# Kernel optimization log

Hardware: AMD Instinct MI355X
Metric: run time of the kernel (lower is better)

Reference implementation:

```python
import jax, jax.numpy as jnp
import numpy as np
import math

L, K, B = 16, 2048, 2
BATCH = 4
N = K * B


def _pe(k, b_beats):
    # PositionalEncoding buffer: pe[features_dim=K, num_of_beats=B]
    pos = jnp.arange(k, dtype=jnp.float32)[:, None]                      # (K, 1)
    div = jnp.exp(jnp.arange(0, b_beats, 2, dtype=jnp.float32) * (-math.log(10000.0) / b_beats))
    pe = jnp.zeros((k, b_beats), dtype=jnp.float32)
    pe = pe.at[:, 0::2].set(jnp.sin(pos * div))
    pe = pe.at[:, 1::2].set(jnp.cos(pos * div))
    return pe                                                            # (K, B)


def setup_inputs() -> dict:
    key = jax.random.key(0)
    ks = jax.random.split(key, 10)
    return {
        "X": jax.random.normal(ks[0], (BATCH, L, N), jnp.float32),
        "S": jax.random.normal(ks[1], (BATCH, L, N), jnp.float32),
        "W_1x": jax.random.normal(ks[2], (L, L), jnp.float32),
        "W_1s": jax.random.normal(ks[3], (L, L), jnp.float32),
        "W_2x": jax.random.normal(ks[4], (K, K), jnp.float32),
        "W_2s": jax.random.normal(ks[5], (K, K), jnp.float32),
        "conv_wx": jax.random.normal(ks[6], (2 * L, 2 * L, 3, 3), jnp.float32) * 0.05,
        "conv_bx": jnp.zeros((2 * L,), jnp.float32),
        "conv_ws": jax.random.normal(ks[7], (2 * L, 2 * L, 3, 3), jnp.float32) * 0.05,
        "conv_bs": jnp.zeros((2 * L,), jnp.float32),
    }


def _branch(E, W2):
    # E: (b, L, N). A = softmax(E^T E, axis=2); Ea = E @ A; then K-dim mixing by W2.
    b = E.shape[0]
    A = jax.nn.softmax(jnp.einsum('bln,blm->bnm', E, E), axis=2)         # (b, N, N)
    Ea = jnp.einsum('bln,bnm->blm', E, A)                                # (b, L, N)
    Ea4 = Ea.reshape(b, L, K, B)
    M = jnp.einsum('blkt,kj->bljt', Ea4, W2)                             # (b, L, K, B)
    return M.reshape(b, L, N)


def _conv(x, w, bias):
    y = jax.lax.conv_general_dilated(x, w, (1, 1), 'SAME',
                                     dimension_numbers=('NCHW', 'OIHW', 'NCHW'))
    return y + bias[None, :, None, None]


def reference(X, S, W_1x, W_1s, W_2x, W_2s, conv_wx, conv_bx, conv_ws, conv_bs):
    b = X.shape[0]
    Xe = jnp.einsum('bln,lm->bmn', S, W_1x)
    Se = jnp.einsum('bln,lm->bmn', X, W_1s)
    Mx = _branch(Xe, W_2x)
    Ms = _branch(Se, W_2s)
    X_hat = jnp.concatenate((Mx * X, X), axis=1).reshape(b, 2 * L, K, B)
    S_hat = jnp.concatenate((Ms * S, S), axis=1).reshape(b, 2 * L, K, B)
    # positional encoding broadcast over (batch, 2L); dropout in eval mode = identity
    S_hat = S_hat + _pe(K, B)[None, None]
    X_e_hat = _conv(X_hat, conv_wx, conv_bx)
    S_e_hat = _conv(S_hat, conv_ws, conv_bs)
    return jnp.concatenate((X_e_hat, S_e_hat), axis=1)                   # (b, 4L, K, B)
```

## Files before the change

### kernel.cpp

```cpp
#include <hip/hip_runtime.h>
#include <math.h>

#define TPB 256

static constexpr int LL = 16;
static constexpr int KK = 2048;
static constexpr int NBATCH = 4;
static constexpr int NN = 4096;
static constexpr int BBR = 8;

static constexpr size_t OFF_EHL = 0;
static constexpr size_t OFF_ET  = 524288;
static constexpr size_t OFF_LSE = 786432;
static constexpr size_t OFF_EAT = 819200;
static constexpr size_t OFF_XH  = 1081344;
static constexpr size_t OFF_SH  = 1605632;
static constexpr size_t OFF_PB  = 2129920;
static constexpr size_t OFF_PMX = 3178496;
static constexpr size_t OFF_PSM = 3244032;

typedef unsigned short ushortT;
typedef __attribute__((ext_vector_type(8))) short short8v;
typedef __attribute__((ext_vector_type(4))) float f32x4;

__device__ __forceinline__ ushortT f2bf(float x) {
  union { float f; unsigned int u; } c; c.f = x;
  unsigned int u = c.u;
  return (ushortT)((u + 0x7FFFu + ((u >> 16) & 1u)) >> 16);
}
__device__ __forceinline__ float bf2f(ushortT h) {
  union { unsigned int u; float f; } c; c.u = ((unsigned int)h) << 16;
  return c.f;
}
__device__ __forceinline__ float exp2a(float x) {
  float r; asm("v_exp_f32 %0, %1" : "=v"(r) : "v"(x)); return r;
}

__global__ __launch_bounds__(TPB) void prep_kernel(
    const float* __restrict__ X, const float* __restrict__ S,
    const float* __restrict__ W1x, const float* __restrict__ W1s,
    ushortT* __restrict__ Ehl, ushortT* __restrict__ Ept) {
  __shared__ float wsh[256];
  __shared__ ushortT tl[16][272];
  const int tid = threadIdx.x;
  const int br = blockIdx.z;
  wsh[tid] = br ? W1s[tid] : W1x[tid];
  __syncthreads();
  const int n0 = blockIdx.x * 256;
  const int b = blockIdx.y;
  const int n = n0 + tid;
  const float SC = 1.2011224087f;
  const int wq = tid & 31;
  const int slot = (wq < 16) ? ((wq >> 2) * 8 + (wq & 3))
                             : (((wq - 16) >> 2) * 8 + 4 + (wq & 3));
  const int ptid = (tid & ~31) | slot;
  const float* In = br ? X : S;

  float in[16];
#pragma unroll
  for (int l = 0; l < 16; ++l)
    in[l] = In[(size_t)(b * 16 + l) * NN + n];
  float e[16];
#pragma unroll
  for (int m = 0; m < 16; ++m) {
    float a0 = 0.f;
#pragma unroll
    for (int l = 0; l < 16; ++l) a0 = fmaf(in[l], wsh[l * 16 + m], a0);
    e[m] = a0;
  }
  const int bbr = br * 4 + b;
  unsigned int rw[16];
#pragma unroll
  for (int q = 0; q < 16; ++q) rw[q] = 0;
#pragma unroll
  for (int k = 0; k < 16; ++k) {
    const float vs = e[k] * SC;
    ushortT h = f2bf(vs);
    ushortT lo = f2bf(vs - bf2f(h));
    rw[k >> 1] |= ((unsigned int)h) << (16 * (k & 1));
    rw[8 + (k >> 1)] |= ((unsigned int)lo) << (16 * (k & 1));
    tl[k][ptid] = f2bf(e[k]);
  }
  uint4* dst = (uint4*)(Ehl + ((size_t)bbr * NN + n) * 32);
  dst[0] = make_uint4(rw[0], rw[1], rw[2], rw[3]);
  dst[1] = make_uint4(rw[4], rw[5], rw[6], rw[7]);
  dst[2] = make_uint4(rw[8], rw[9], rw[10], rw[11]);
  dst[3] = make_uint4(rw[12], rw[13], rw[14], rw[15]);
  __syncthreads();
  {
    const int r = tid >> 4, c0 = (tid & 15) * 16;
    const uint4* src = (const uint4*)(&tl[r][c0]);
    uint4* d2 = (uint4*)(Ept + ((size_t)bbr * 16 + r) * NN + n0 + c0);
    d2[0] = src[0];
    d2[1] = src[1];
  }
}

__global__ __launch_bounds__(TPB) void passA_kernel(
    const ushortT* __restrict__ Ehl, float* __restrict__ pmx,
    float* __restrict__ psm) {
  const int bid = blockIdx.x;
  const int bbr = bid & 7;
  const int ms = (bid >> 3) & 1;
  const int n0 = (bid >> 4) * 32;
  const int tid = threadIdx.x;
  const int w = tid >> 6, lane = tid & 63;
  const int lr = lane & 15, g = lane >> 4;
  const ushortT* Eb = Ehl + (size_t)bbr * NN * 32;

  const short8v zero8 = {0, 0, 0, 0, 0, 0, 0, 0};
  short8v b1[2], b2[2];
#pragma unroll
  for (int s = 0; s < 2; ++s) {
    const ushortT* rp = Eb + (size_t)(n0 + s * 16 + lr) * 32;
    b1[s] = *(const short8v*)(rp + (g & 1) * 8);
    b2[s] = zero8;
    if (g < 2) b2[s] = *(const short8v*)(rp + 16 + g * 8);
  }
  float mx[2] = {-INFINITY, -INFINITY};
  float sm[2] = {0.f, 0.f};
  const f32x4 z = {0.f, 0.f, 0.f, 0.f};
  const ushortT* ap = Eb + (size_t)(ms * 2048 + w * 512 + lr) * 32 + g * 8;
#pragma unroll 2
  for (int ch = 0; ch < 16; ++ch) {
    short8v a0 = *(const short8v*)ap;
    short8v a1 = *(const short8v*)(ap + 16 * 32);
    ap += 32 * 32;
#pragma unroll
    for (int s = 0; s < 2; ++s) {
      f32x4 c0 = __builtin_amdgcn_mfma_f32_16x16x32_bf16(a0, b1[s], z, 0, 0, 0);
      c0 = __builtin_amdgcn_mfma_f32_16x16x32_bf16(a0, b2[s], c0, 0, 0, 0);
      f32x4 c1 = __builtin_amdgcn_mfma_f32_16x16x32_bf16(a1, b1[s], z, 0, 0, 0);
      c1 = __builtin_amdgcn_mfma_f32_16x16x32_bf16(a1, b2[s], c1, 0, 0, 0);
      float t0 = fmaxf(fmaxf(c0[0], c0[1]), fmaxf(c0[2], c0[3]));
      float t1 = fmaxf(fmaxf(c1[0], c1[1]), fmaxf(c1[2], c1[3]));
      float tm = fmaxf(t0, t1);
      if (tm > mx[s] + 30.f) {
        sm[s] *= exp2a(mx[s] - tm);
        mx[s] = tm;
      }
      float e0 = exp2a(c0[0] - mx[s]), e1 = exp2a(c0[1] - mx[s]);
      float e2 = exp2a(c0[2] - mx[s]), e3 = exp2a(c0[3] - mx[s]);
      float e4 = exp2a(c1[0] - mx[s]), e5 = exp2a(c1[1] - mx[s]);
      float e6 = exp2a(c1[2] - mx[s]), e7 = exp2a(c1[3] - mx[s]);
      sm[s] += ((e0 + e1) + (e2 + e3)) + ((e4 + e5) + (e6 + e7));
    }
  }
#pragma unroll
  for (int s = 0; s < 2; ++s) {
    for (int off = 16; off < 64; off <<= 1) {
      float omx = __shfl_xor(mx[s], off);
      float osm = __shfl_xor(sm[s], off);
      float nm = fmaxf(mx[s], omx);
      sm[s] = sm[s] * exp2a(mx[s] - nm) + osm * exp2a(omx - nm);
      mx[s] = nm;
    }
  }
  __shared__ float smx[4][2][16], ssm[4][2][16];
  if (lane < 16) {
    smx[w][0][lr] = mx[0]; ssm[w][0][lr] = sm[0];
    smx[w][1][lr] = mx[1]; ssm[w][1][lr] = sm[1];
  }
  __syncthreads();
  if (tid < 32) {
    const int s = tid >> 4, col = tid & 15;
    float M = fmaxf(fmaxf(smx[0][s][col], smx[1][s][col]),
                    fmaxf(smx[2][s][col], smx[3][s][col]));
    float Ssum = ssm[0][s][col] * exp2a(smx[0][s][col] - M) +
                 ssm[1][s][col] * exp2a(smx[1][s][col] - M) +
                 ssm[2][s][col] * exp2a(smx[2][s][col] - M) +
                 ssm[3][s][col] * exp2a(smx[3][s][col] - M);
    const size_t o = (size_t)(ms * 8 + bbr) * NN + n0 + s * 16 + col;
    pmx[o] = M;
    psm[o] = Ssum;
  }
}

__global__ __launch_bounds__(TPB) void reduceA_kernel(
    const float* __restrict__ pmx, const float* __restrict__ psm,
    float* __restrict__ nlse) {
  const int idx = blockIdx.x * TPB + threadIdx.x;
  float m0 = pmx[idx], m1 = pmx[32768 + idx];
  float s0 = psm[idx], s1 = psm[32768 + idx];
  float M = fmaxf(m0, m1);
  float S = s0 * exp2a(m0 - M) + s1 * exp2a(m1 - M);
  nlse[idx] = -(M + log2f(fmaxf(S, 1e-38f)));
}

__global__ __launch_bounds__(TPB) void passB_kernel(
    const ushortT* __restrict__ Ehl, const ushortT* __restrict__ Ept,
    const float* __restrict__ nlse, float* __restrict__ pb) {
  const int bid = blockIdx.x;
  const int bbr = bid & 7;
  const int ns = (bid >> 3) & 1;
  const int m0 = (bid >> 4) * 64;
  const int tid = threadIdx.x;
  const int w = tid >> 6, lane = tid & 63;
  const int lr = lane & 15, g = lane >> 4;
  const ushortT* Eb = Ehl + (size_t)bbr * NN * 32;
  const ushortT* Tb = Ept + (size_t)bbr * 16 * NN;
  __shared__ float lsb[2048];
  __shared__ float red[4][4][16][17];
  for (int i = tid; i < 2048; i += TPB)
    lsb[i] = nlse[(size_t)bbr * NN + ns * 2048 + i];
  __syncthreads();

  const short8v zero8 = {0, 0, 0, 0, 0, 0, 0, 0};
  short8v b1[4], b2[4];
#pragma unroll
  for (int s = 0; s < 4; ++s) {
    const ushortT* rp = Eb + (size_t)(m0 + s * 16 + lr) * 32;
    b1[s] = *(const short8v*)(rp + (g & 1) * 8);
    b2[s] = zero8;
    if (g < 2) b2[s] = *(const short8v*)(rp + 16 + g * 8);
  }
  f32x4 acc[4] = {{0.f, 0.f, 0.f, 0.f}, {0.f, 0.f, 0.f, 0.f},
                  {0.f, 0.f, 0.f, 0.f}, {0.f, 0.f, 0.f, 0.f}};
  const ushortT* ap = Eb + (size_t)(ns * 2048 + w * 512 + lr) * 32 + g * 8;
  const ushortT* vp = Tb + (size_t)lr * NN + ns * 2048 + w * 512 + g * 8;
  const float* lp = lsb + w * 512 + g * 4;
#pragma unroll 2
  for (int ch = 0; ch < 16; ++ch) {
    short8v a0 = *(const short8v*)ap;
    short8v a1 = *(const short8v*)(ap + 16 * 32);
    short8v ae = *(const short8v*)vp;
    f32x4 sd0 = *(const f32x4*)lp;
    f32x4 sd1 = *(const f32x4*)(lp + 16);
    ap += 32 * 32; vp += 32; lp += 32;
#pragma unroll
    for (int s = 0; s < 4; ++s) {
      f32x4 c0 = __builtin_amdgcn_mfma_f32_16x16x32_bf16(a0, b1[s], sd0, 0, 0, 0);
      c0 = __builtin_amdgcn_mfma_f32_16x16x32_bf16(a0, b2[s], c0, 0, 0, 0);
      f32x4 c1 = __builtin_amdgcn_mfma_f32_16x16x32_bf16(a1, b1[s], sd1, 0, 0, 0);
      c1 = __builtin_amdgcn_mfma_f32_16x16x32_bf16(a1, b2[s], c1, 0, 0, 0);
      float p0 = exp2a(c0[0]), p1 = exp2a(c0[1]);
      float p2 = exp2a(c0[2]), p3 = exp2a(c0[3]);
      float q0 = exp2a(c1[0]), q1 = exp2a(c1[1]);
      float q2 = exp2a(c1[2]), q3 = exp2a(c1[3]);
      unsigned int u0, u1, u2, u3;
      asm("v_cvt_pk_bf16_f32 %0, %1, %2" : "=v"(u0) : "v"(p0), "v"(p1));
      asm("v_cvt_pk_bf16_f32 %0, %1, %2" : "=v"(u1) : "v"(p2), "v"(p3));
      asm("v_cvt_pk_bf16_f32 %0, %1, %2" : "=v"(u2) : "v"(q0), "v"(q1));
      asm("v_cvt_pk_bf16_f32 %0, %1, %2" : "=v"(u3) : "v"(q2), "v"(q3));
      const uint4 uv = make_uint4(u0, u1, u2, u3);
      const short8v pf = __builtin_bit_cast(short8v, uv);
      acc[s] = __builtin_amdgcn_mfma_f32_16x16x32_bf16(ae, pf, acc[s], 0, 0, 0);
    }
  }
#pragma unroll
  for (int s = 0; s < 4; ++s)
#pragma unroll
    for (int r = 0; r < 4; ++r) red[w][s][g * 4 + r][lr] = acc[s][r];
  __syncthreads();
  for (int o = tid; o < 1024; o += TPB) {
    const int s = o >> 8, l = (o >> 4) & 15, mm = o & 15;
    float v = red[0][s][l][mm] + red[1][s][l][mm] +
              red[2][s][l][mm] + red[3][s][l][mm];
    pb[((size_t)(ns * 8 + bbr) * 16 + l) * NN + m0 + s * 16 + mm] = v;
  }
}

__global__ __launch_bounds__(TPB) void reduceB_kernel(
    const float* __restrict__ pb, ushortT* __restrict__ EaT) {
  const int gidx = blockIdx.x * TPB + threadIdx.x;
  const int r = gidx >> 10;
  const int j4 = gidx & 1023;
  const float4 p0 = *(const float4*)(pb + (size_t)r * NN + j4 * 4);
  const float4 p1 = *(const float4*)(pb + (size_t)(128 + r) * NN + j4 * 4);
  const float v0 = p0.x + p1.x, v1 = p0.y + p1.y;
  const float v2 = p0.z + p1.z, v3 = p0.w + p1.w;
  const int bbr = r >> 4, l = r & 15;
  unsigned int ue, uo;
  asm("v_cvt_pk_bf16_f32 %0, %1, %2" : "=v"(ue) : "v"(v0), "v"(v2));
  asm("v_cvt_pk_bf16_f32 %0, %1, %2" : "=v"(uo) : "v"(v1), "v"(v3));
  *(unsigned int*)(EaT + ((size_t)(bbr * 2 + 0) * 16 + l) * KK + j4 * 2) = ue;
  *(unsigned int*)(EaT + ((size_t)(bbr * 2 + 1) * 16 + l) * KK + j4 * 2) = uo;
}

__global__ __launch_bounds__(TPB) void mmix_kernel(
    const ushortT* __restrict__ EaT,
    const float* __restrict__ W2x, const float* __restrict__ W2s,
    const float* __restrict__ X, const float* __restrict__ S,
    float* __restrict__ Xhat, float* __restrict__ Shat) {
  const int jt = blockIdx.x;
  const int br = blockIdx.y;
  const float* W2 = br ? W2s : W2x;
  const int j0 = jt * 16;
  const int tid = threadIdx.x;
  const int w = tid >> 6, lane = tid & 63;
  const int b = w;
  const int lj = tid & 15, kp0 = tid >> 4;
  const int fl = lane & 15, g = lane >> 4;
  __shared__ ushortT bpan[2][16][72];

  const size_t rb0 = ((size_t)(br * 4 + b) * 2 + 0) * 16;
  const size_t rb1 = ((size_t)(br * 4 + b) * 2 + 1) * 16;

  f32x4 acc0 = {0.f, 0.f, 0.f, 0.f};
  f32x4 acc1 = {0.f, 0.f, 0.f, 0.f};

  float r0, r1, r2, r3;
  r0 = W2[(size_t)(2 * kp0)      * KK + j0 + lj];
  r1 = W2[(size_t)(2 * kp0 + 1)  * KK + j0 + lj];
  r2 = W2[(size_t)(2 * kp0 + 32) * KK + j0 + lj];
  r3 = W2[(size_t)(2 * kp0 + 33) * KK + j0 + lj];

  for (int c = 0; c < 32; ++c) {
    const int cur = c & 1;
    unsigned int u0, u1;
    asm("v_cvt_pk_bf16_f32 %0, %1, %2" : "=v"(u0) : "v"(r0), "v"(r1));
    asm("v_cvt_pk_bf16_f32 %0, %1, %2" : "=v"(u1) : "v"(r2), "v"(r3));
    *(unsigned int*)(&bpan[cur][lj][kp0 * 2]) = u0;
    *(unsigned int*)(&bpan[cur][lj][(kp0 + 16) * 2]) = u1;
    __syncthreads();
    if (c < 31) {
      const int kc = (c + 1) * 64;
      r0 = W2[(size_t)(kc + 2 * kp0)      * KK + j0 + lj];
      r1 = W2[(size_t)(kc + 2 * kp0 + 1)  * KK + j0 + lj];
      r2 = W2[(size_t)(kc + 2 * kp0 + 32) * KK + j0 + lj];
      r3 = W2[(size_t)(kc + 2 * kp0 + 33) * KK + j0 + lj];
    }
#pragma unroll
    for (int s = 0; s < 2; ++s) {
      const int k = c * 64 + s * 32 + g * 8;
      short8v bf = *(const short8v*)(&bpan[cur][fl][s * 32 + g * 8]);
      short8v a0 = *(const short8v*)(EaT + (rb0 + fl) * (size_t)KK + k);
      short8v a1 = *(const short8v*)(EaT + (rb1 + fl) * (size_t)KK + k);
      acc0 = __builtin_amdgcn_mfma_f32_16x16x32_bf16(a0, bf, acc0, 0, 0, 0);
      acc1 = __builtin_amdgcn_mfma_f32_16x16x32_bf16(a1, bf, acc1, 0, 0, 0);
    }
    __syncthreads();
  }

  const int j = j0 + fl;
#pragma unroll
  for (int r = 0; r < 4; ++r) {
    const int l = g * 4 + r;
    if (br == 0) {
      float xv0 = X[(size_t)(b * 16 + l) * NN + 2 * j + 0];
      Xhat[((size_t)(b * 32 + l) * KK + j) * 2 + 0] = acc0[r] * xv0;
      Xhat[((size_t)(b * 32 + 16 + l) * KK + j) * 2 + 0] = xv0;
      float xv1 = X[(size_t)(b * 16 + l) * NN + 2 * j + 1];
      Xhat[((size_t)(b * 32 + l) * KK + j) * 2 + 1] = acc1[r] * xv1;
      Xhat[((size_t)(b * 32 + 16 + l) * KK + j) * 2 + 1] = xv1;
    } else {
      float pe0 = sinf((float)j), pe1 = cosf((float)j);
      float sv0 = S[(size_t)(b * 16 + l) * NN + 2 * j + 0];
      Shat[((size_t)(b * 32 + l) * KK + j) * 2 + 0] = fmaf(acc0[r], sv0, pe0);
      Shat[((size_t)(b * 32 + 16 + l) * KK + j) * 2 + 0] = sv0 + pe0;
      float sv1 = S[(size_t)(b * 16 + l) * NN + 2 * j + 1];
      Shat[((size_t)(b * 32 + l) * KK + j) * 2 + 1] = fmaf(acc1[r], sv1, pe1);
      Shat[((size_t)(b * 32 + 16 + l) * KK + j) * 2 + 1] = sv1 + pe1;
    }
  }
}

__global__ __launch_bounds__(TPB) void conv_kernel(
    const float* __restrict__ Xhat, const float* __restrict__ Shat,
    const float* __restrict__ Wx, const float* __restrict__ Bx,
    const float* __restrict__ Ws, const float* __restrict__ Bs,
    float* __restrict__ out) {
  const int kt = blockIdx.x;
  const int b = blockIdx.y;
  const int br = blockIdx.z;
  const float* In = (br ? Shat : Xhat) + (size_t)b * 32 * KK * 2;
  const float* Wt = br ? Ws : Wx;
  const float* Bi = br ? Bs : Bx;
  __shared__ float inT[32 * 34 * 2];
  __shared__ float wts[32 * 289];
  const int tid = threadIdx.x;
  const int k0 = kt * 32;

  for (int f = tid; f < 32 * 288; f += TPB) {
    const int c = f / 288, rem = f % 288;
    wts[c * 289 + rem] = Wt[f];
  }
  for (int f = tid; f < 32 * 34 * 2; f += TPB) {
    const int ch = f / 68, rem = f % 68;
    const int kk = rem >> 1, t = rem & 1;
    const int kg = k0 - 1 + kk;
    inT[f] = (kg >= 0 && kg < KK) ? In[((size_t)ch * KK + kg) * 2 + t] : 0.f;
  }
  __syncthreads();

  const int c = tid >> 3, sub = tid & 7;
  const float bias = Bi[c];
  float acc0[4], acc1[4];
#pragma unroll
  for (int i = 0; i < 4; ++i) { acc0[i] = bias; acc1[i] = bias; }

  for (int cin = 0; cin < 32; ++cin) {
    const float* wp = wts + c * 289 + cin * 9;
    const float w00 = wp[0], w01 = wp[1], w02 = wp[2];
    const float w10 = wp[3], w11 = wp[4], w12 = wp[5];
    const float w20 = wp[6], w21 = wp[7], w22 = wp[8];
    const float* ip = inT + cin * 68;
#pragma unroll
    for (int i = 0; i < 4; ++i) {
      const int kl = sub + 8 * i;
      const float* q = ip + kl * 2;
      const float i00 = q[0], i01 = q[1];
      const float i10 = q[2], i11 = q[3];
      const float i20 = q[4], i21 = q[5];
      acc0[i] = fmaf(i00, w01, acc0[i]); acc0[i] = fmaf(i01, w02, acc0[i]);
      acc0[i] = fmaf(i10, w11, acc0[i]); acc0[i] = fmaf(i11, w12, acc0[i]);
      acc0[i] = fmaf(i20, w21, acc0[i]); acc0[i] = fmaf(i21, w22, acc0[i]);
      acc1[i] = fmaf(i00, w00, acc1[i]); acc1[i] = fmaf(i01, w01, acc1[i]);
      acc1[i] = fmaf(i10, w10, acc1[i]); acc1[i] = fmaf(i11, w11, acc1[i]);
      acc1[i] = fmaf(i20, w20, acc1[i]); acc1[i] = fmaf(i21, w21, acc1[i]);
    }
  }
#pragma unroll
  for (int i = 0; i < 4; ++i) {
    const int k = k0 + sub + 8 * i;
    const size_t o = ((size_t)(b * 64 + br * 32 + c) * KK + k) * 2;
    out[o] = acc0[i];
    out[o + 1] = acc1[i];
  }
}

extern "C" void kernel_launch(void* const* d_in, const int* in_sizes, int n_in,
                              void* d_out, int out_size, void* d_ws, size_t ws_size,
                              hipStream_t stream) {
  (void)in_sizes; (void)n_in; (void)out_size; (void)ws_size;
  const float* X   = (const float*)d_in[0];
  const float* S   = (const float*)d_in[1];
  const float* W1x = (const float*)d_in[2];
  const float* W1s = (const float*)d_in[3];
  const float* W2x = (const float*)d_in[4];
  const float* W2s = (const float*)d_in[5];
  const float* Cwx = (const float*)d_in[6];
  const float* Cbx = (const float*)d_in[7];
  const float* Cws = (const float*)d_in[8];
  const float* Cbs = (const float*)d_in[9];
  float* out = (float*)d_out;
  float* ws = (float*)d_ws;

  ushortT* Ehl = (ushortT*)(ws + OFF_EHL);
  ushortT* Ept = (ushortT*)(ws + OFF_ET);
  float*   nls = ws + OFF_LSE;
  ushortT* EaT = (ushortT*)(ws + OFF_EAT);
  float*   Xh  = ws + OFF_XH;
  float*   Sh  = ws + OFF_SH;
  float*   pb  = ws + OFF_PB;
  float*   pmx = ws + OFF_PMX;
  float*   psm = ws + OFF_PSM;

  hipLaunchKernelGGL(prep_kernel, dim3(16, NBATCH, 2), dim3(TPB), 0, stream,
                     X, S, W1x, W1s, Ehl, Ept);
  hipLaunchKernelGGL(passA_kernel, dim3(2048), dim3(TPB), 0, stream,
                     Ehl, pmx, psm);
  hipLaunchKernelGGL(reduceA_kernel, dim3(128), dim3(TPB), 0, stream,
                     pmx, psm, nls);
  hipLaunchKernelGGL(passB_kernel, dim3(1024), dim3(TPB), 0, stream,
                     Ehl, Ept, nls, pb);
  hipLaunchKernelGGL(reduceB_kernel, dim3(512), dim3(TPB), 0, stream,
                     pb, EaT);
  hipLaunchKernelGGL(mmix_kernel, dim3(128, 2), dim3(TPB), 0, stream,
                     EaT, W2x, W2s, X, S, Xh, Sh);
  hipLaunchKernelGGL(conv_kernel, dim3(64, NBATCH, 2), dim3(TPB), 0, stream,
                     Xh, Sh, Cwx, Cbx, Cws, Cbs, out);
}
```

Before: 125.7 us.

## Split-K the W2 mixing GEMM and widen passA column tiles

The mmix kernel now splits the K=2048 reduction into four slices across a new grid dimension, which raises its grid from 256 to 1024 blocks. Each slice writes fp32 partials to a new workspace region, and a new mergeM kernel sums them and applies the X/S multiply and positional-encoding epilogue. Separately, passA blocks now each process 64 columns instead of 32, halving the block count and reusing each A-fragment load across four column tiles. The cost is an extra launch plus partial-sum traffic, and passA holds more live registers.

```diff
diff --git a/kernel.cpp b/kernel.cpp
--- a/kernel.cpp
+++ b/kernel.cpp
@@ -18,6 +18,7 @@
 static constexpr size_t OFF_PB  = 2129920;
 static constexpr size_t OFF_PMX = 3178496;
 static constexpr size_t OFF_PSM = 3244032;
+static constexpr size_t OFF_PMM = 3309568;
 
 typedef unsigned short ushortT;
 typedef __attribute__((ext_vector_type(8))) short short8v;
@@ -102,23 +103,23 @@
   const int bid = blockIdx.x;
   const int bbr = bid & 7;
   const int ms = (bid >> 3) & 1;
-  const int n0 = (bid >> 4) * 32;
+  const int n0 = (bid >> 4) * 64;
   const int tid = threadIdx.x;
   const int w = tid >> 6, lane = tid & 63;
   const int lr = lane & 15, g = lane >> 4;
   const ushortT* Eb = Ehl + (size_t)bbr * NN * 32;
 
   const short8v zero8 = {0, 0, 0, 0, 0, 0, 0, 0};
-  short8v b1[2], b2[2];
-#pragma unroll
-  for (int s = 0; s < 2; ++s) {
+  short8v b1[4], b2[4];
+#pragma unroll
+  for (int s = 0; s < 4; ++s) {
     const ushortT* rp = Eb + (size_t)(n0 + s * 16 + lr) * 32;
     b1[s] = *(const short8v*)(rp + (g & 1) * 8);
     b2[s] = zero8;
     if (g < 2) b2[s] = *(const short8v*)(rp + 16 + g * 8);
   }
-  float mx[2] = {-INFINITY, -INFINITY};
-  float sm[2] = {0.f, 0.f};
+  float mx[4] = {-INFINITY, -INFINITY, -INFINITY, -INFINITY};
+  float sm[4] = {0.f, 0.f, 0.f, 0.f};
   const f32x4 z = {0.f, 0.f, 0.f, 0.f};
   const ushortT* ap = Eb + (size_t)(ms * 2048 + w * 512 + lr) * 32 + g * 8;
 #pragma unroll 2
@@ -127,7 +128,7 @@
     short8v a1 = *(const short8v*)(ap + 16 * 32);
     ap += 32 * 32;
 #pragma unroll
-    for (int s = 0; s < 2; ++s) {
+    for (int s = 0; s < 4; ++s) {
       f32x4 c0 = __builtin_amdgcn_mfma_f32_16x16x32_bf16(a0, b1[s], z, 0, 0, 0);
       c0 = __builtin_amdgcn_mfma_f32_16x16x32_bf16(a0, b2[s], c0, 0, 0, 0);
       f32x4 c1 = __builtin_amdgcn_mfma_f32_16x16x32_bf16(a1, b1[s], z, 0, 0, 0);
@@ -147,7 +148,7 @@
     }
   }
 #pragma unroll
-  for (int s = 0; s < 2; ++s) {
+  for (int s = 0; s < 4; ++s) {
     for (int off = 16; off < 64; off <<= 1) {
       float omx = __shfl_xor(mx[s], off);
       float osm = __shfl_xor(sm[s], off);
@@ -156,13 +157,16 @@
       mx[s] = nm;
     }
   }
-  __shared__ float smx[4][2][16], ssm[4][2][16];
+  __shared__ float smx[4][4][16], ssm[4][4][16];
   if (lane < 16) {
-    smx[w][0][lr] = mx[0]; ssm[w][0][lr] = sm[0];
-    smx[w][1][lr] = mx[1]; ssm[w][1][lr] = sm[1];
-  }
-  __syncthreads();
-  if (tid < 32) {
+#pragma unroll
+    for (int s = 0; s < 4; ++s) {
+      smx[w][s][lr] = mx[s];
+      ssm[w][s][lr] = sm[s];
+    }
+  }
+  __syncthreads();
+  if (tid < 64) {
     const int s = tid >> 4, col = tid & 15;
     float M = fmaxf(fmaxf(smx[0][s][col], smx[1][s][col]),
                     fmaxf(smx[2][s][col], smx[3][s][col]));
@@ -280,12 +284,13 @@
 __global__ __launch_bounds__(TPB) void mmix_kernel(
     const ushortT* __restrict__ EaT,
     const float* __restrict__ W2x, const float* __restrict__ W2s,
-    const float* __restrict__ X, const float* __restrict__ S,
-    float* __restrict__ Xhat, float* __restrict__ Shat) {
+    float* __restrict__ pmm) {
   const int jt = blockIdx.x;
   const int br = blockIdx.y;
+  const int ks = blockIdx.z;
   const float* W2 = br ? W2s : W2x;
   const int j0 = jt * 16;
+  const int kb = ks * 512;
   const int tid = threadIdx.x;
   const int w = tid >> 6, lane = tid & 63;
   const int b = w;
@@ -300,12 +305,12 @@
   f32x4 acc1 = {0.f, 0.f, 0.f, 0.f};
 
   float r0, r1, r2, r3;
-  r0 = W2[(size_t)(2 * kp0)      * KK + j0 + lj];
-  r1 = W2[(size_t)(2 * kp0 + 1)  * KK + j0 + lj];
-  r2 = W2[(size_t)(2 * kp0 + 32) * KK + j0 + lj];
-  r3 = W2[(size_t)(2 * kp0 + 33) * KK + j0 + lj];
-
-  for (int c = 0; c < 32; ++c) {
+  r0 = W2[(size_t)(kb + 2 * kp0)      * KK + j0 + lj];
+  r1 = W2[(size_t)(kb + 2 * kp0 + 1)  * KK + j0 + lj];
+  r2 = W2[(size_t)(kb + 2 * kp0 + 32) * KK + j0 + lj];
+  r3 = W2[(size_t)(kb + 2 * kp0 + 33) * KK + j0 + lj];
+
+  for (int c = 0; c < 8; ++c) {
     const int cur = c & 1;
     unsigned int u0, u1;
     asm("v_cvt_pk_bf16_f32 %0, %1, %2" : "=v"(u0) : "v"(r0), "v"(r1));
@@ -313,8 +318,8 @@
     *(unsigned int*)(&bpan[cur][lj][kp0 * 2]) = u0;
     *(unsigned int*)(&bpan[cur][lj][(kp0 + 16) * 2]) = u1;
     __syncthreads();
-    if (c < 31) {
-      const int kc = (c + 1) * 64;
+    if (c < 7) {
+      const int kc = kb + (c + 1) * 64;
       r0 = W2[(size_t)(kc + 2 * kp0)      * KK + j0 + lj];
       r1 = W2[(size_t)(kc + 2 * kp0 + 1)  * KK + j0 + lj];
       r2 = W2[(size_t)(kc + 2 * kp0 + 32) * KK + j0 + lj];
@@ -322,7 +327,7 @@
     }
 #pragma unroll
     for (int s = 0; s < 2; ++s) {
-      const int k = c * 64 + s * 32 + g * 8;
+      const int k = kb + c * 64 + s * 32 + g * 8;
       short8v bf = *(const short8v*)(&bpan[cur][fl][s * 32 + g * 8]);
       short8v a0 = *(const short8v*)(EaT + (rb0 + fl) * (size_t)KK + k);
       short8v a1 = *(const short8v*)(EaT + (rb1 + fl) * (size_t)KK + k);
@@ -336,20 +341,47 @@
 #pragma unroll
   for (int r = 0; r < 4; ++r) {
     const int l = g * 4 + r;
+    const size_t base = ((size_t)(ks * 2 + br) * 4 + b) * 2;
+    pmm[((base + 0) * 16 + l) * (size_t)KK + j] = acc0[r];
+    pmm[((base + 1) * 16 + l) * (size_t)KK + j] = acc1[r];
+  }
+}
+
+__global__ __launch_bounds__(TPB) void mergeM_kernel(
+    const float* __restrict__ pmm,
+    const float* __restrict__ X, const float* __restrict__ S,
+    float* __restrict__ Xhat, float* __restrict__ Shat) {
+  const int jt = blockIdx.x;
+  const int br = blockIdx.y;
+  const int tid = threadIdx.x;
+  const int w = tid >> 6, lane = tid & 63;
+  const int b = w;
+  const int fl = lane & 15, g = lane >> 4;
+  const int j = jt * 16 + fl;
+#pragma unroll
+  for (int r = 0; r < 4; ++r) {
+    const int l = g * 4 + r;
+    float a0 = 0.f, a1 = 0.f;
+#pragma unroll
+    for (int ks = 0; ks < 4; ++ks) {
+      const size_t base = ((size_t)(ks * 2 + br) * 4 + b) * 2;
+      a0 += pmm[((base + 0) * 16 + l) * (size_t)KK + j];
+      a1 += pmm[((base + 1) * 16 + l) * (size_t)KK + j];
+    }
     if (br == 0) {
       float xv0 = X[(size_t)(b * 16 + l) * NN + 2 * j + 0];
-      Xhat[((size_t)(b * 32 + l) * KK + j) * 2 + 0] = acc0[r] * xv0;
+      Xhat[((size_t)(b * 32 + l) * KK + j) * 2 + 0] = a0 * xv0;
       Xhat[((size_t)(b * 32 + 16 + l) * KK + j) * 2 + 0] = xv0;
       float xv1 = X[(size_t)(b * 16 + l) * NN + 2 * j + 1];
-      Xhat[((size_t)(b * 32 + l) * KK + j) * 2 + 1] = acc1[r] * xv1;
+      Xhat[((size_t)(b * 32 + l) * KK + j) * 2 + 1] = a1 * xv1;
       Xhat[((size_t)(b * 32 + 16 + l) * KK + j) * 2 + 1] = xv1;
     } else {
       float pe0 = sinf((float)j), pe1 = cosf((float)j);
       float sv0 = S[(size_t)(b * 16 + l) * NN + 2 * j + 0];
-      Shat[((size_t)(b * 32 + l) * KK + j) * 2 + 0] = fmaf(acc0[r], sv0, pe0);
+      Shat[((size_t)(b * 32 + l) * KK + j) * 2 + 0] = fmaf(a0, sv0, pe0);
       Shat[((size_t)(b * 32 + 16 + l) * KK + j) * 2 + 0] = sv0 + pe0;
       float sv1 = S[(size_t)(b * 16 + l) * NN + 2 * j + 1];
-      Shat[((size_t)(b * 32 + l) * KK + j) * 2 + 1] = fmaf(acc1[r], sv1, pe1);
+      Shat[((size_t)(b * 32 + l) * KK + j) * 2 + 1] = fmaf(a1, sv1, pe1);
       Shat[((size_t)(b * 32 + 16 + l) * KK + j) * 2 + 1] = sv1 + pe1;
     }
   }
@@ -445,10 +477,11 @@
   float*   pb  = ws + OFF_PB;
   float*   pmx = ws + OFF_PMX;
   float*   psm = ws + OFF_PSM;
+  float*   pmm = ws + OFF_PMM;
 
   hipLaunchKernelGGL(prep_kernel, dim3(16, NBATCH, 2), dim3(TPB), 0, stream,
                      X, S, W1x, W1s, Ehl, Ept);
-  hipLaunchKernelGGL(passA_kernel, dim3(2048), dim3(TPB), 0, stream,
+  hipLaunchKernelGGL(passA_kernel, dim3(1024), dim3(TPB), 0, stream,
                      Ehl, pmx, psm);
   hipLaunchKernelGGL(reduceA_kernel, dim3(128), dim3(TPB), 0, stream,
                      pmx, psm, nls);
@@ -456,8 +489,10 @@
                      Ehl, Ept, nls, pb);
   hipLaunchKernelGGL(reduceB_kernel, dim3(512), dim3(TPB), 0, stream,
                      pb, EaT);
-  hipLaunchKernelGGL(mmix_kernel, dim3(128, 2), dim3(TPB), 0, stream,
-                     EaT, W2x, W2s, X, S, Xh, Sh);
+  hipLaunchKernelGGL(mmix_kernel, dim3(128, 2, 4), dim3(TPB), 0, stream,
+                     EaT, W2x, W2s, pmm);
+  hipLaunchKernelGGL(mergeM_kernel, dim3(128, 2), dim3(TPB), 0, stream,
+                     pmm, X, S, Xh, Sh);
   hipLaunchKernelGGL(conv_kernel, dim3(64, NBATCH, 2), dim3(TPB), 0, stream,
                      Xh, Sh, Cwx, Cbx, Cws, Cbs, out);
 }
```

After: 114.7 us. 8.7% less time.
